# Kernel tuning notes

Hardware: AMD Instinct MI355X
Metric: run time of the kernel (lower is better)

Reference implementation:

```python
import jax, jax.numpy as jnp
import numpy as np

D = 64  # hidden_dim


def _bn(x, gamma, beta):
    # eval-mode BatchNorm1d with running_mean=0, running_var=1 (fresh model)
    return gamma * x + beta


def _edge_conv(h, W, b, gamma, beta):
    # h: [B,N,D]; W: [2D,D] split into Wi (acts on x_i) and Wj (acts on x_j)
    Wi, Wj = W[:D], W[D:]
    ti = jnp.einsum('bnd,de->bne', h, Wi)  # [B,N,D] (i term)
    tj = jnp.einsum('bmd,de->bme', h, Wj)  # [B,N,D] (j term)
    # e[b,i,j,:] = x_i@Wi + x_j@Wj + b  -> relu -> BN -> max over j
    e = ti[:, :, None, :] + tj[:, None, :, :] + b  # [B,N,N,D]
    e = _bn(jax.nn.relu(e), gamma, beta)
    return e.max(axis=2)  # [B,N,D]


def setup_inputs() -> dict:
    key = jax.random.key(0)
    ks = jax.random.split(key, 16)
    s = lambda k, shp, sc: (jax.random.normal(k, shp, dtype=jnp.float32) * sc)
    inp = {
        'x': s(ks[0], (32, 256, 4), 1.0),
        'W1': s(ks[1], (4, D), 0.5), 'b1': s(ks[2], (D,), 0.1),
        'g1': 1.0 + s(ks[3], (D,), 0.1), 'beta1': s(ks[4], (D,), 0.1),
        'We1': s(ks[5], (2 * D, D), 0.1), 'be1': s(ks[6], (D,), 0.1),
        'ge1': 1.0 + s(ks[7], (D,), 0.1), 'betae1': s(ks[8], (D,), 0.1),
        'We2': s(ks[9], (2 * D, D), 0.1), 'be2': s(ks[10], (D,), 0.1),
        'ge2': 1.0 + s(ks[11], (D,), 0.1), 'betae2': s(ks[12], (D,), 0.1),
        'Wg1': s(ks[13], (2 * D, D), 0.1), 'bg1': s(ks[14], (D,), 0.1),
        'Wg2': s(ks[15], (D, 2), 0.1), 'bg2': jnp.zeros((2,), jnp.float32),
    }
    return inp


def reference(x, W1, b1, g1, beta1, We1, be1, ge1, betae1, We2, be2, ge2, betae2, Wg1, bg1, Wg2, bg2):
    # input MLP: Linear -> ReLU -> BN (eval)
    h = _bn(jax.nn.relu(x @ W1 + b1), g1, beta1)  # [B,N,D]
    h = _edge_conv(h, We1, be1, ge1, betae1)
    h = _edge_conv(h, We2, be2, ge2, betae2)
    x_mean = h.mean(axis=1)  # [B,D]
    x_max = h.max(axis=1)    # [B,D]
    xg = jnp.concatenate([x_mean, x_max], axis=-1)  # [B,2D]
    # global MLP (dropout is identity in eval)
    out = jax.nn.relu(xg @ Wg1 + bg1) @ Wg2 + bg2  # [B,2]
    return out
```

## Files before the change

kernel.cpp:

```cpp
#include <hip/hip_runtime.h>

#define NB 32
#define NN 256
#define DD 64
#define GG 4
#define NPB 64
#define FMAXV 3.402823466e+38f


__global__ __launch_bounds__(512) void k_conv1(
    const float* __restrict__ x,
    const float* __restrict__ W1,  const float* __restrict__ b1,
    const float* __restrict__ g1,  const float* __restrict__ beta1,
    const float* __restrict__ We1,
    float* __restrict__ TI, float* __restrict__ PMAX, float* __restrict__ PMIN)
{
    __shared__ float Hs[NPB * 65];
    const int b  = blockIdx.x >> 2;
    const int g  = blockIdx.x & 3;
    const int l  = threadIdx.x & 63;
    const int w  = __builtin_amdgcn_readfirstlane(threadIdx.x >> 6);
    const int n  = g * NPB + l;
    const int d0 = w * 8;

    {
        float4 xv = *(const float4*)(x + ((size_t)b * NN + n) * 4);
        float a[8];
#pragma unroll
        for (int j = 0; j < 8; ++j) a[j] = b1[d0 + j];
#pragma unroll
        for (int j = 0; j < 8; ++j) a[j] = fmaf(xv.x, W1[0 * DD + d0 + j], a[j]);
#pragma unroll
        for (int j = 0; j < 8; ++j) a[j] = fmaf(xv.y, W1[1 * DD + d0 + j], a[j]);
#pragma unroll
        for (int j = 0; j < 8; ++j) a[j] = fmaf(xv.z, W1[2 * DD + d0 + j], a[j]);
#pragma unroll
        for (int j = 0; j < 8; ++j) a[j] = fmaf(xv.w, W1[3 * DD + d0 + j], a[j]);
#pragma unroll
        for (int j = 0; j < 8; ++j)
            Hs[l * 65 + d0 + j] = g1[d0 + j] * fmaxf(a[j], 0.f) + beta1[d0 + j];
    }
    __syncthreads();

    float ti[8], tj[8];
#pragma unroll
    for (int j = 0; j < 8; ++j) { ti[j] = 0.f; tj[j] = 0.f; }
#pragma unroll
    for (int k = 0; k < DD; ++k) {
        const float hk = Hs[l * 65 + k];
        const float* wi = We1 + k * DD + d0;
        const float* wj = We1 + (DD + k) * DD + d0;
#pragma unroll
        for (int j = 0; j < 8; ++j) {
            ti[j] = fmaf(hk, wi[j], ti[j]);
            tj[j] = fmaf(hk, wj[j], tj[j]);
        }
    }
    {
        float* o = TI + ((size_t)(b * NN + n)) * DD + d0;
        *(float4*)(o)     = make_float4(ti[0], ti[1], ti[2], ti[3]);
        *(float4*)(o + 4) = make_float4(ti[4], ti[5], ti[6], ti[7]);
    }
    float mx[8], mn[8];
#pragma unroll
    for (int j = 0; j < 8; ++j) { mx[j] = tj[j]; mn[j] = tj[j]; }
#pragma unroll
    for (int m = 1; m < 64; m <<= 1) {
#pragma unroll
        for (int j = 0; j < 8; ++j) {
            mx[j] = fmaxf(mx[j], __shfl_xor(mx[j], m, 64));
            mn[j] = fminf(mn[j], __shfl_xor(mn[j], m, 64));
        }
    }
    float smx = mx[0], smn = mn[0];
#pragma unroll
    for (int j = 1; j < 8; ++j) {
        smx = (l == j) ? mx[j] : smx;
        smn = (l == j) ? mn[j] : smn;
    }
    if (l < 8) {
        PMAX[(b * GG + g) * DD + d0 + l] = smx;
        PMIN[(b * GG + g) * DD + d0 + l] = smn;
    }
}

__global__ __launch_bounds__(512) void k_conv2(
    const float* __restrict__ PMAXin, const float* __restrict__ PMINin,
    const float* __restrict__ beP, const float* __restrict__ geP,
    const float* __restrict__ bteP,
    const float* __restrict__ We,
    float* __restrict__ TI, float* __restrict__ PMAX, float* __restrict__ PMIN)
{
    __shared__ float Hs[NPB * 65];
    const int b  = blockIdx.x >> 2;
    const int g  = blockIdx.x & 3;
    const int l  = threadIdx.x & 63;
    const int w  = __builtin_amdgcn_readfirstlane(threadIdx.x >> 6);
    const int n  = g * NPB + l;
    const int d0 = w * 8;

    float rmax[8], rmin[8];
#pragma unroll
    for (int j = 0; j < 8; ++j) {
        rmax[j] = fmaxf(fmaxf(PMAXin[(b * GG + 0) * DD + d0 + j],
                              PMAXin[(b * GG + 1) * DD + d0 + j]),
                        fmaxf(PMAXin[(b * GG + 2) * DD + d0 + j],
                              PMAXin[(b * GG + 3) * DD + d0 + j]));
        rmin[j] = fminf(fminf(PMINin[(b * GG + 0) * DD + d0 + j],
                              PMINin[(b * GG + 1) * DD + d0 + j]),
                        fminf(PMINin[(b * GG + 2) * DD + d0 + j],
                              PMINin[(b * GG + 3) * DD + d0 + j]));
    }
    {
        const float* tip = TI + ((size_t)(b * NN + n)) * DD + d0;
        float4 t0 = *(const float4*)tip;
        float4 t1 = *(const float4*)(tip + 4);
        float tiv[8] = {t0.x, t0.y, t0.z, t0.w, t1.x, t1.y, t1.z, t1.w};
#pragma unroll
        for (int j = 0; j < 8; ++j) {
            float gv = geP[d0 + j];
            float sv = tiv[j] + (gv >= 0.f ? rmax[j] : rmin[j]) + beP[d0 + j];
            Hs[l * 65 + d0 + j] = gv * fmaxf(sv, 0.f) + bteP[d0 + j];
        }
    }
    __syncthreads();

    float ti[8], tj[8];
#pragma unroll
    for (int j = 0; j < 8; ++j) { ti[j] = 0.f; tj[j] = 0.f; }
#pragma unroll
    for (int k = 0; k < DD; ++k) {
        const float hk = Hs[l * 65 + k];
        const float* wi = We + k * DD + d0;
        const float* wj = We + (DD + k) * DD + d0;
#pragma unroll
        for (int j = 0; j < 8; ++j) {
            ti[j] = fmaf(hk, wi[j], ti[j]);
            tj[j] = fmaf(hk, wj[j], tj[j]);
        }
    }
    {
        float* o = TI + ((size_t)(b * NN + n)) * DD + d0;
        *(float4*)(o)     = make_float4(ti[0], ti[1], ti[2], ti[3]);
        *(float4*)(o + 4) = make_float4(ti[4], ti[5], ti[6], ti[7]);
    }
    float mx[8], mn[8];
#pragma unroll
    for (int j = 0; j < 8; ++j) { mx[j] = tj[j]; mn[j] = tj[j]; }
#pragma unroll
    for (int m = 1; m < 64; m <<= 1) {
#pragma unroll
        for (int j = 0; j < 8; ++j) {
            mx[j] = fmaxf(mx[j], __shfl_xor(mx[j], m, 64));
            mn[j] = fminf(mn[j], __shfl_xor(mn[j], m, 64));
        }
    }
    float smx = mx[0], smn = mn[0];
#pragma unroll
    for (int j = 1; j < 8; ++j) {
        smx = (l == j) ? mx[j] : smx;
        smn = (l == j) ? mn[j] : smn;
    }
    if (l < 8) {
        PMAX[(b * GG + g) * DD + d0 + l] = smx;
        PMIN[(b * GG + g) * DD + d0 + l] = smn;
    }
}

__global__ __launch_bounds__(512) void k_pool(
    const float* __restrict__ PMAXin, const float* __restrict__ PMINin,
    const float* __restrict__ beP, const float* __restrict__ geP,
    const float* __restrict__ bteP,
    const float* __restrict__ TI,
    float* __restrict__ PSUM, float* __restrict__ PMXP)
{
    const int b  = blockIdx.x >> 2;
    const int g  = blockIdx.x & 3;
    const int l  = threadIdx.x & 63;
    const int w  = __builtin_amdgcn_readfirstlane(threadIdx.x >> 6);
    const int n  = g * NPB + l;
    const int d0 = w * 8;

    float rmax[8], rmin[8];
#pragma unroll
    for (int j = 0; j < 8; ++j) {
        rmax[j] = fmaxf(fmaxf(PMAXin[(b * GG + 0) * DD + d0 + j],
                              PMAXin[(b * GG + 1) * DD + d0 + j]),
                        fmaxf(PMAXin[(b * GG + 2) * DD + d0 + j],
                              PMAXin[(b * GG + 3) * DD + d0 + j]));
        rmin[j] = fminf(fminf(PMINin[(b * GG + 0) * DD + d0 + j],
                              PMINin[(b * GG + 1) * DD + d0 + j]),
                        fminf(PMINin[(b * GG + 2) * DD + d0 + j],
                              PMINin[(b * GG + 3) * DD + d0 + j]));
    }
    float hv[8];
    {
        const float* tip = TI + ((size_t)(b * NN + n)) * DD + d0;
        float4 t0 = *(const float4*)tip;
        float4 t1 = *(const float4*)(tip + 4);
        float tiv[8] = {t0.x, t0.y, t0.z, t0.w, t1.x, t1.y, t1.z, t1.w};
#pragma unroll
        for (int j = 0; j < 8; ++j) {
            float gv = geP[d0 + j];
            float sv = tiv[j] + (gv >= 0.f ? rmax[j] : rmin[j]) + beP[d0 + j];
            hv[j] = gv * fmaxf(sv, 0.f) + bteP[d0 + j];
        }
    }
    float sm[8], mx[8];
#pragma unroll
    for (int j = 0; j < 8; ++j) { sm[j] = hv[j]; mx[j] = hv[j]; }
#pragma unroll
    for (int m = 1; m < 64; m <<= 1) {
#pragma unroll
        for (int j = 0; j < 8; ++j) {
            sm[j] += __shfl_xor(sm[j], m, 64);
            mx[j] = fmaxf(mx[j], __shfl_xor(mx[j], m, 64));
        }
    }
    float ssm = sm[0], smx = mx[0];
#pragma unroll
    for (int j = 1; j < 8; ++j) {
        ssm = (l == j) ? sm[j] : ssm;
        smx = (l == j) ? mx[j] : smx;
    }
    if (l < 8) {
        PSUM[(b * GG + g) * DD + d0 + l] = ssm;
        PMXP[(b * GG + g) * DD + d0 + l] = smx;
    }
}

__global__ __launch_bounds__(128) void k_head(
    const float* __restrict__ PSUM, const float* __restrict__ PMXP,
    const float* __restrict__ Wg1, const float* __restrict__ bg1,
    const float* __restrict__ Wg2, const float* __restrict__ bg2,
    float* __restrict__ out)
{
    __shared__ float xg[2 * DD];
    __shared__ float hid[DD];
    const int b = blockIdx.x;
    const int t = threadIdx.x;
    if (t < 64) {
        float s = PSUM[(b * GG + 0) * DD + t] + PSUM[(b * GG + 1) * DD + t]
                + PSUM[(b * GG + 2) * DD + t] + PSUM[(b * GG + 3) * DD + t];
        xg[t] = s * (1.f / 256.f);
    } else {
        int d = t - 64;
        xg[64 + d] = fmaxf(fmaxf(PMXP[(b * GG + 0) * DD + d], PMXP[(b * GG + 1) * DD + d]),
                           fmaxf(PMXP[(b * GG + 2) * DD + d], PMXP[(b * GG + 3) * DD + d]));
    }
    __syncthreads();
    if (t < 64) {
        float a = bg1[t];
#pragma unroll
        for (int k = 0; k < 2 * DD; ++k) a = fmaf(xg[k], Wg1[k * DD + t], a);
        hid[t] = fmaxf(a, 0.f);
    }
    __syncthreads();
    if (t < 2) {
        float o = bg2[t];
#pragma unroll
        for (int j = 0; j < DD; ++j) o = fmaf(hid[j], Wg2[j * 2 + t], o);
        out[b * 2 + t] = o;
    }
}

extern "C" void kernel_launch(void* const* d_in, const int* in_sizes, int n_in,
                              void* d_out, int out_size, void* d_ws, size_t ws_size,
                              hipStream_t stream) {
    const float* x     = (const float*)d_in[0];
    const float* W1    = (const float*)d_in[1];
    const float* b1    = (const float*)d_in[2];
    const float* g1    = (const float*)d_in[3];
    const float* beta1 = (const float*)d_in[4];
    const float* We1   = (const float*)d_in[5];
    const float* be1   = (const float*)d_in[6];
    const float* ge1   = (const float*)d_in[7];
    const float* bte1  = (const float*)d_in[8];
    const float* We2   = (const float*)d_in[9];
    const float* be2   = (const float*)d_in[10];
    const float* ge2   = (const float*)d_in[11];
    const float* bte2  = (const float*)d_in[12];
    const float* Wg1   = (const float*)d_in[13];
    const float* bg1   = (const float*)d_in[14];
    const float* Wg2   = (const float*)d_in[15];
    const float* bg2   = (const float*)d_in[16];

    float* ws    = (float*)d_ws;
    float* TI    = ws;
    float* PMAX1 = ws + 524288;
    float* PMIN1 = ws + 532480;
    float* PMAX2 = ws + 540672;
    float* PMIN2 = ws + 548864;
    float* PSUM  = ws + 557056;
    float* PMXP  = ws + 565248;

    k_conv1<<<dim3(NB * GG), dim3(512), 0, stream>>>(
        x, W1, b1, g1, beta1, We1, TI, PMAX1, PMIN1);
    k_conv2<<<dim3(NB * GG), dim3(512), 0, stream>>>(
        PMAX1, PMIN1, be1, ge1, bte1, We2, TI, PMAX2, PMIN2);
    k_pool<<<dim3(NB * GG), dim3(512), 0, stream>>>(
        PMAX2, PMIN2, be2, ge2, bte2, TI, PSUM, PMXP);
    k_head<<<dim3(NB), dim3(128), 0, stream>>>(
        PSUM, PMXP, Wg1, bg1, Wg2, bg2, (float*)d_out);
}
```

Baseline: 121.4 us.

## Fuse all stages into one cooperative kernel with grid syncs

Replaces four separate kernel launches with a single cooperative kernel that uses grid-wide synchronization between stages. The per-node ti term stays in registers across stages instead of round-tripping through the TI workspace buffer. This removes launch gaps and global traffic, but adds grid.sync costs and requires all 128 blocks to be co-resident.

```diff
diff --git a/kernel.cpp b/kernel.cpp
--- a/kernel.cpp
+++ b/kernel.cpp
@@ -1,27 +1,48 @@
 #include <hip/hip_runtime.h>
+#include <hip/hip_cooperative_groups.h>
+
+namespace cg = cooperative_groups;
 
 #define NB 32
 #define NN 256
 #define DD 64
 #define GG 4
 #define NPB 64
-#define FMAXV 3.402823466e+38f
-
-
-__global__ __launch_bounds__(512) void k_conv1(
+#define NBLK (NB * GG)
+
+
+__global__ __launch_bounds__(512, 1) void pnet_coop(
     const float* __restrict__ x,
     const float* __restrict__ W1,  const float* __restrict__ b1,
     const float* __restrict__ g1,  const float* __restrict__ beta1,
-    const float* __restrict__ We1,
-    float* __restrict__ TI, float* __restrict__ PMAX, float* __restrict__ PMIN)
+    const float* __restrict__ We1, const float* __restrict__ be1,
+    const float* __restrict__ ge1, const float* __restrict__ bte1,
+    const float* __restrict__ We2, const float* __restrict__ be2,
+    const float* __restrict__ ge2, const float* __restrict__ bte2,
+    const float* __restrict__ Wg1, const float* __restrict__ bg1,
+    const float* __restrict__ Wg2, const float* __restrict__ bg2,
+    float* __restrict__ PM, float* __restrict__ out)
 {
+    cg::grid_group grid = cg::this_grid();
+
     __shared__ float Hs[NPB * 65];
-    const int b  = blockIdx.x >> 2;
-    const int g  = blockIdx.x & 3;
-    const int l  = threadIdx.x & 63;
-    const int w  = __builtin_amdgcn_readfirstlane(threadIdx.x >> 6);
-    const int n  = g * NPB + l;
-    const int d0 = w * 8;
+    __shared__ float XG[2 * DD];
+    __shared__ float HID[DD];
+
+    float* PMAX1 = PM;
+    float* PMIN1 = PM + 8192;
+    float* PMAX2 = PM + 16384;
+    float* PMIN2 = PM + 24576;
+    float* PSUM  = PM + 32768;
+    float* PMXP  = PM + 40960;
+
+    const int bid = blockIdx.x;
+    const int b   = bid >> 2;
+    const int g   = bid & 3;
+    const int l   = threadIdx.x & 63;
+    const int w   = __builtin_amdgcn_readfirstlane(threadIdx.x >> 6);
+    const int n   = g * NPB + l;
+    const int d0  = w * 8;
 
     {
         float4 xv = *(const float4*)(x + ((size_t)b * NN + n) * 4);
@@ -42,225 +63,176 @@
     }
     __syncthreads();
 
-    float ti[8], tj[8];
-#pragma unroll
-    for (int j = 0; j < 8; ++j) { ti[j] = 0.f; tj[j] = 0.f; }
-#pragma unroll
-    for (int k = 0; k < DD; ++k) {
-        const float hk = Hs[l * 65 + k];
-        const float* wi = We1 + k * DD + d0;
-        const float* wj = We1 + (DD + k) * DD + d0;
-#pragma unroll
-        for (int j = 0; j < 8; ++j) {
-            ti[j] = fmaf(hk, wi[j], ti[j]);
-            tj[j] = fmaf(hk, wj[j], tj[j]);
-        }
-    }
-    {
-        float* o = TI + ((size_t)(b * NN + n)) * DD + d0;
-        *(float4*)(o)     = make_float4(ti[0], ti[1], ti[2], ti[3]);
-        *(float4*)(o + 4) = make_float4(ti[4], ti[5], ti[6], ti[7]);
-    }
-    float mx[8], mn[8];
-#pragma unroll
-    for (int j = 0; j < 8; ++j) { mx[j] = tj[j]; mn[j] = tj[j]; }
-#pragma unroll
-    for (int m = 1; m < 64; m <<= 1) {
-#pragma unroll
-        for (int j = 0; j < 8; ++j) {
-            mx[j] = fmaxf(mx[j], __shfl_xor(mx[j], m, 64));
-            mn[j] = fminf(mn[j], __shfl_xor(mn[j], m, 64));
-        }
-    }
-    float smx = mx[0], smn = mn[0];
-#pragma unroll
-    for (int j = 1; j < 8; ++j) {
-        smx = (l == j) ? mx[j] : smx;
-        smn = (l == j) ? mn[j] : smn;
-    }
-    if (l < 8) {
-        PMAX[(b * GG + g) * DD + d0 + l] = smx;
-        PMIN[(b * GG + g) * DD + d0 + l] = smn;
-    }
-}
-
-__global__ __launch_bounds__(512) void k_conv2(
-    const float* __restrict__ PMAXin, const float* __restrict__ PMINin,
-    const float* __restrict__ beP, const float* __restrict__ geP,
-    const float* __restrict__ bteP,
-    const float* __restrict__ We,
-    float* __restrict__ TI, float* __restrict__ PMAX, float* __restrict__ PMIN)
-{
-    __shared__ float Hs[NPB * 65];
-    const int b  = blockIdx.x >> 2;
-    const int g  = blockIdx.x & 3;
-    const int l  = threadIdx.x & 63;
-    const int w  = __builtin_amdgcn_readfirstlane(threadIdx.x >> 6);
-    const int n  = g * NPB + l;
-    const int d0 = w * 8;
-
-    float rmax[8], rmin[8];
-#pragma unroll
-    for (int j = 0; j < 8; ++j) {
-        rmax[j] = fmaxf(fmaxf(PMAXin[(b * GG + 0) * DD + d0 + j],
-                              PMAXin[(b * GG + 1) * DD + d0 + j]),
-                        fmaxf(PMAXin[(b * GG + 2) * DD + d0 + j],
-                              PMAXin[(b * GG + 3) * DD + d0 + j]));
-        rmin[j] = fminf(fminf(PMINin[(b * GG + 0) * DD + d0 + j],
-                              PMINin[(b * GG + 1) * DD + d0 + j]),
-                        fminf(PMINin[(b * GG + 2) * DD + d0 + j],
-                              PMINin[(b * GG + 3) * DD + d0 + j]));
-    }
-    {
-        const float* tip = TI + ((size_t)(b * NN + n)) * DD + d0;
-        float4 t0 = *(const float4*)tip;
-        float4 t1 = *(const float4*)(tip + 4);
-        float tiv[8] = {t0.x, t0.y, t0.z, t0.w, t1.x, t1.y, t1.z, t1.w};
-#pragma unroll
-        for (int j = 0; j < 8; ++j) {
-            float gv = geP[d0 + j];
-            float sv = tiv[j] + (gv >= 0.f ? rmax[j] : rmin[j]) + beP[d0 + j];
-            Hs[l * 65 + d0 + j] = gv * fmaxf(sv, 0.f) + bteP[d0 + j];
-        }
-    }
-    __syncthreads();
-
-    float ti[8], tj[8];
-#pragma unroll
-    for (int j = 0; j < 8; ++j) { ti[j] = 0.f; tj[j] = 0.f; }
-#pragma unroll
-    for (int k = 0; k < DD; ++k) {
-        const float hk = Hs[l * 65 + k];
-        const float* wi = We + k * DD + d0;
-        const float* wj = We + (DD + k) * DD + d0;
-#pragma unroll
-        for (int j = 0; j < 8; ++j) {
-            ti[j] = fmaf(hk, wi[j], ti[j]);
-            tj[j] = fmaf(hk, wj[j], tj[j]);
-        }
-    }
-    {
-        float* o = TI + ((size_t)(b * NN + n)) * DD + d0;
-        *(float4*)(o)     = make_float4(ti[0], ti[1], ti[2], ti[3]);
-        *(float4*)(o + 4) = make_float4(ti[4], ti[5], ti[6], ti[7]);
-    }
-    float mx[8], mn[8];
-#pragma unroll
-    for (int j = 0; j < 8; ++j) { mx[j] = tj[j]; mn[j] = tj[j]; }
-#pragma unroll
-    for (int m = 1; m < 64; m <<= 1) {
-#pragma unroll
-        for (int j = 0; j < 8; ++j) {
-            mx[j] = fmaxf(mx[j], __shfl_xor(mx[j], m, 64));
-            mn[j] = fminf(mn[j], __shfl_xor(mn[j], m, 64));
-        }
-    }
-    float smx = mx[0], smn = mn[0];
-#pragma unroll
-    for (int j = 1; j < 8; ++j) {
-        smx = (l == j) ? mx[j] : smx;
-        smn = (l == j) ? mn[j] : smn;
-    }
-    if (l < 8) {
-        PMAX[(b * GG + g) * DD + d0 + l] = smx;
-        PMIN[(b * GG + g) * DD + d0 + l] = smn;
-    }
-}
-
-__global__ __launch_bounds__(512) void k_pool(
-    const float* __restrict__ PMAXin, const float* __restrict__ PMINin,
-    const float* __restrict__ beP, const float* __restrict__ geP,
-    const float* __restrict__ bteP,
-    const float* __restrict__ TI,
-    float* __restrict__ PSUM, float* __restrict__ PMXP)
-{
-    const int b  = blockIdx.x >> 2;
-    const int g  = blockIdx.x & 3;
-    const int l  = threadIdx.x & 63;
-    const int w  = __builtin_amdgcn_readfirstlane(threadIdx.x >> 6);
-    const int n  = g * NPB + l;
-    const int d0 = w * 8;
-
-    float rmax[8], rmin[8];
-#pragma unroll
-    for (int j = 0; j < 8; ++j) {
-        rmax[j] = fmaxf(fmaxf(PMAXin[(b * GG + 0) * DD + d0 + j],
-                              PMAXin[(b * GG + 1) * DD + d0 + j]),
-                        fmaxf(PMAXin[(b * GG + 2) * DD + d0 + j],
-                              PMAXin[(b * GG + 3) * DD + d0 + j]));
-        rmin[j] = fminf(fminf(PMINin[(b * GG + 0) * DD + d0 + j],
-                              PMINin[(b * GG + 1) * DD + d0 + j]),
-                        fminf(PMINin[(b * GG + 2) * DD + d0 + j],
-                              PMINin[(b * GG + 3) * DD + d0 + j]));
-    }
-    float hv[8];
-    {
-        const float* tip = TI + ((size_t)(b * NN + n)) * DD + d0;
-        float4 t0 = *(const float4*)tip;
-        float4 t1 = *(const float4*)(tip + 4);
-        float tiv[8] = {t0.x, t0.y, t0.z, t0.w, t1.x, t1.y, t1.z, t1.w};
-#pragma unroll
-        for (int j = 0; j < 8; ++j) {
-            float gv = geP[d0 + j];
-            float sv = tiv[j] + (gv >= 0.f ? rmax[j] : rmin[j]) + beP[d0 + j];
-            hv[j] = gv * fmaxf(sv, 0.f) + bteP[d0 + j];
-        }
-    }
-    float sm[8], mx[8];
-#pragma unroll
-    for (int j = 0; j < 8; ++j) { sm[j] = hv[j]; mx[j] = hv[j]; }
-#pragma unroll
-    for (int m = 1; m < 64; m <<= 1) {
-#pragma unroll
-        for (int j = 0; j < 8; ++j) {
-            sm[j] += __shfl_xor(sm[j], m, 64);
-            mx[j] = fmaxf(mx[j], __shfl_xor(mx[j], m, 64));
-        }
-    }
-    float ssm = sm[0], smx = mx[0];
-#pragma unroll
-    for (int j = 1; j < 8; ++j) {
-        ssm = (l == j) ? sm[j] : ssm;
-        smx = (l == j) ? mx[j] : smx;
-    }
-    if (l < 8) {
-        PSUM[(b * GG + g) * DD + d0 + l] = ssm;
-        PMXP[(b * GG + g) * DD + d0 + l] = smx;
-    }
-}
-
-__global__ __launch_bounds__(128) void k_head(
-    const float* __restrict__ PSUM, const float* __restrict__ PMXP,
-    const float* __restrict__ Wg1, const float* __restrict__ bg1,
-    const float* __restrict__ Wg2, const float* __restrict__ bg2,
-    float* __restrict__ out)
-{
-    __shared__ float xg[2 * DD];
-    __shared__ float hid[DD];
-    const int b = blockIdx.x;
-    const int t = threadIdx.x;
-    if (t < 64) {
-        float s = PSUM[(b * GG + 0) * DD + t] + PSUM[(b * GG + 1) * DD + t]
-                + PSUM[(b * GG + 2) * DD + t] + PSUM[(b * GG + 3) * DD + t];
-        xg[t] = s * (1.f / 256.f);
-    } else {
-        int d = t - 64;
-        xg[64 + d] = fmaxf(fmaxf(PMXP[(b * GG + 0) * DD + d], PMXP[(b * GG + 1) * DD + d]),
-                           fmaxf(PMXP[(b * GG + 2) * DD + d], PMXP[(b * GG + 3) * DD + d]));
-    }
-    __syncthreads();
-    if (t < 64) {
-        float a = bg1[t];
-#pragma unroll
-        for (int k = 0; k < 2 * DD; ++k) a = fmaf(xg[k], Wg1[k * DD + t], a);
-        hid[t] = fmaxf(a, 0.f);
-    }
-    __syncthreads();
-    if (t < 2) {
-        float o = bg2[t];
-#pragma unroll
-        for (int j = 0; j < DD; ++j) o = fmaf(hid[j], Wg2[j * 2 + t], o);
-        out[b * 2 + t] = o;
+    float ti1[8];
+    {
+        float tj[8];
+#pragma unroll
+        for (int j = 0; j < 8; ++j) { ti1[j] = 0.f; tj[j] = 0.f; }
+#pragma unroll
+        for (int k = 0; k < DD; ++k) {
+            const float hk = Hs[l * 65 + k];
+            const float* wi = We1 + k * DD + d0;
+            const float* wj = We1 + (DD + k) * DD + d0;
+#pragma unroll
+            for (int j = 0; j < 8; ++j) {
+                ti1[j] = fmaf(hk, wi[j], ti1[j]);
+                tj[j]  = fmaf(hk, wj[j], tj[j]);
+            }
+        }
+        float mx[8], mn[8];
+#pragma unroll
+        for (int j = 0; j < 8; ++j) { mx[j] = tj[j]; mn[j] = tj[j]; }
+#pragma unroll
+        for (int m = 1; m < 64; m <<= 1) {
+#pragma unroll
+            for (int j = 0; j < 8; ++j) {
+                mx[j] = fmaxf(mx[j], __shfl_xor(mx[j], m, 64));
+                mn[j] = fminf(mn[j], __shfl_xor(mn[j], m, 64));
+            }
+        }
+        float smx = mx[0], smn = mn[0];
+#pragma unroll
+        for (int j = 1; j < 8; ++j) {
+            smx = (l == j) ? mx[j] : smx;
+            smn = (l == j) ? mn[j] : smn;
+        }
+        if (l < 8) {
+            PMAX1[(b * GG + g) * DD + d0 + l] = smx;
+            PMIN1[(b * GG + g) * DD + d0 + l] = smn;
+        }
+    }
+    grid.sync();
+
+    float ti2[8];
+    {
+        float rmax[8], rmin[8];
+#pragma unroll
+        for (int j = 0; j < 8; ++j) {
+            rmax[j] = fmaxf(fmaxf(PMAX1[(b * GG + 0) * DD + d0 + j],
+                                  PMAX1[(b * GG + 1) * DD + d0 + j]),
+                            fmaxf(PMAX1[(b * GG + 2) * DD + d0 + j],
+                                  PMAX1[(b * GG + 3) * DD + d0 + j]));
+            rmin[j] = fminf(fminf(PMIN1[(b * GG + 0) * DD + d0 + j],
+                                  PMIN1[(b * GG + 1) * DD + d0 + j]),
+                            fminf(PMIN1[(b * GG + 2) * DD + d0 + j],
+                                  PMIN1[(b * GG + 3) * DD + d0 + j]));
+        }
+        __syncthreads();
+#pragma unroll
+        for (int j = 0; j < 8; ++j) {
+            float gv = ge1[d0 + j];
+            float sv = ti1[j] + (gv >= 0.f ? rmax[j] : rmin[j]) + be1[d0 + j];
+            Hs[l * 65 + d0 + j] = gv * fmaxf(sv, 0.f) + bte1[d0 + j];
+        }
+        __syncthreads();
+
+        float tj[8];
+#pragma unroll
+        for (int j = 0; j < 8; ++j) { ti2[j] = 0.f; tj[j] = 0.f; }
+#pragma unroll
+        for (int k = 0; k < DD; ++k) {
+            const float hk = Hs[l * 65 + k];
+            const float* wi = We2 + k * DD + d0;
+            const float* wj = We2 + (DD + k) * DD + d0;
+#pragma unroll
+            for (int j = 0; j < 8; ++j) {
+                ti2[j] = fmaf(hk, wi[j], ti2[j]);
+                tj[j]  = fmaf(hk, wj[j], tj[j]);
+            }
+        }
+        float mx[8], mn[8];
+#pragma unroll
+        for (int j = 0; j < 8; ++j) { mx[j] = tj[j]; mn[j] = tj[j]; }
+#pragma unroll
+        for (int m = 1; m < 64; m <<= 1) {
+#pragma unroll
+            for (int j = 0; j < 8; ++j) {
+                mx[j] = fmaxf(mx[j], __shfl_xor(mx[j], m, 64));
+                mn[j] = fminf(mn[j], __shfl_xor(mn[j], m, 64));
+            }
+        }
+        float smx = mx[0], smn = mn[0];
+#pragma unroll
+        for (int j = 1; j < 8; ++j) {
+            smx = (l == j) ? mx[j] : smx;
+            smn = (l == j) ? mn[j] : smn;
+        }
+        if (l < 8) {
+            PMAX2[(b * GG + g) * DD + d0 + l] = smx;
+            PMIN2[(b * GG + g) * DD + d0 + l] = smn;
+        }
+    }
+    grid.sync();
+
+    {
+        float rmax[8], rmin[8];
+#pragma unroll
+        for (int j = 0; j < 8; ++j) {
+            rmax[j] = fmaxf(fmaxf(PMAX2[(b * GG + 0) * DD + d0 + j],
+                                  PMAX2[(b * GG + 1) * DD + d0 + j]),
+                            fmaxf(PMAX2[(b * GG + 2) * DD + d0 + j],
+                                  PMAX2[(b * GG + 3) * DD + d0 + j]));
+            rmin[j] = fminf(fminf(PMIN2[(b * GG + 0) * DD + d0 + j],
+                                  PMIN2[(b * GG + 1) * DD + d0 + j]),
+                            fminf(PMIN2[(b * GG + 2) * DD + d0 + j],
+                                  PMIN2[(b * GG + 3) * DD + d0 + j]));
+        }
+        float hv[8];
+#pragma unroll
+        for (int j = 0; j < 8; ++j) {
+            float gv = ge2[d0 + j];
+            float sv = ti2[j] + (gv >= 0.f ? rmax[j] : rmin[j]) + be2[d0 + j];
+            hv[j] = gv * fmaxf(sv, 0.f) + bte2[d0 + j];
+        }
+        float sm[8], mx[8];
+#pragma unroll
+        for (int j = 0; j < 8; ++j) { sm[j] = hv[j]; mx[j] = hv[j]; }
+#pragma unroll
+        for (int m = 1; m < 64; m <<= 1) {
+#pragma unroll
+            for (int j = 0; j < 8; ++j) {
+                sm[j] += __shfl_xor(sm[j], m, 64);
+                mx[j] = fmaxf(mx[j], __shfl_xor(mx[j], m, 64));
+            }
+        }
+        float ssm = sm[0], smx = mx[0];
+#pragma unroll
+        for (int j = 1; j < 8; ++j) {
+            ssm = (l == j) ? sm[j] : ssm;
+            smx = (l == j) ? mx[j] : smx;
+        }
+        if (l < 8) {
+            PSUM[(b * GG + g) * DD + d0 + l] = ssm;
+            PMXP[(b * GG + g) * DD + d0 + l] = smx;
+        }
+    }
+    grid.sync();
+
+    if (g == 0) {
+        const int t = threadIdx.x;
+        if (t < 64) {
+            float s = PSUM[(b * GG + 0) * DD + t] + PSUM[(b * GG + 1) * DD + t]
+                    + PSUM[(b * GG + 2) * DD + t] + PSUM[(b * GG + 3) * DD + t];
+            XG[t] = s * (1.f / 256.f);
+        } else if (t < 128) {
+            int d = t - 64;
+            XG[64 + d] = fmaxf(fmaxf(PMXP[(b * GG + 0) * DD + d], PMXP[(b * GG + 1) * DD + d]),
+                               fmaxf(PMXP[(b * GG + 2) * DD + d], PMXP[(b * GG + 3) * DD + d]));
+        }
+        __syncthreads();
+        if (t < 64) {
+            float a = bg1[t];
+#pragma unroll
+            for (int k = 0; k < 2 * DD; ++k) a = fmaf(XG[k], Wg1[k * DD + t], a);
+            HID[t] = fmaxf(a, 0.f);
+        }
+        __syncthreads();
+        if (t < 2) {
+            float o = bg2[t];
+#pragma unroll
+            for (int j = 0; j < DD; ++j) o = fmaf(HID[j], Wg2[j * 2 + t], o);
+            out[b * 2 + t] = o;
+        }
     }
 }
 
@@ -284,22 +256,16 @@
     const float* bg1   = (const float*)d_in[14];
     const float* Wg2   = (const float*)d_in[15];
     const float* bg2   = (const float*)d_in[16];
-
-    float* ws    = (float*)d_ws;
-    float* TI    = ws;
-    float* PMAX1 = ws + 524288;
-    float* PMIN1 = ws + 532480;
-    float* PMAX2 = ws + 540672;
-    float* PMIN2 = ws + 548864;
-    float* PSUM  = ws + 557056;
-    float* PMXP  = ws + 565248;
-
-    k_conv1<<<dim3(NB * GG), dim3(512), 0, stream>>>(
-        x, W1, b1, g1, beta1, We1, TI, PMAX1, PMIN1);
-    k_conv2<<<dim3(NB * GG), dim3(512), 0, stream>>>(
-        PMAX1, PMIN1, be1, ge1, bte1, We2, TI, PMAX2, PMIN2);
-    k_pool<<<dim3(NB * GG), dim3(512), 0, stream>>>(
-        PMAX2, PMIN2, be2, ge2, bte2, TI, PSUM, PMXP);
-    k_head<<<dim3(NB), dim3(128), 0, stream>>>(
-        PSUM, PMXP, Wg1, bg1, Wg2, bg2, (float*)d_out);
+    float* PM  = (float*)d_ws;
+    float* out = (float*)d_out;
+
+    void* args[] = {
+        (void*)&x, (void*)&W1, (void*)&b1, (void*)&g1, (void*)&beta1,
+        (void*)&We1, (void*)&be1, (void*)&ge1, (void*)&bte1,
+        (void*)&We2, (void*)&be2, (void*)&ge2, (void*)&bte2,
+        (void*)&Wg1, (void*)&bg1, (void*)&Wg2, (void*)&bg2,
+        (void*)&PM, (void*)&out
+    };
+    hipLaunchCooperativeKernel((void*)pnet_coop, dim3(NBLK), dim3(512),
+                               args, 0, stream);
 }
```

Measured after the change: 204.0 us. +68.1%, slower.

## Fuse pooling and head MLP into one per-batch kernel with LDS reduction

Applied to the files above, without the earlier changes.

Merges the pooling kernel and the global MLP head into a single kernel launched with one block per batch instead of four. Each thread now computes 32 channels for one point and writes them to a padded shared-memory tile, which is then reduced by columns for sum and max before the head MLP runs in the same block. This removes one kernel launch and the global round trip for the partial sums. In exchange it runs only 32 blocks with large shared memory and more registers per thread, so much less of the GPU is occupied.

```diff
diff --git a/kernel.cpp b/kernel.cpp
--- a/kernel.cpp
+++ b/kernel.cpp
@@ -5,7 +5,6 @@
 #define DD 64
 #define GG 4
 #define NPB 64
-#define FMAXV 3.402823466e+38f
 
 
 __global__ __launch_bounds__(512) void k_conv1(
@@ -167,23 +166,32 @@
     }
 }
 
-__global__ __launch_bounds__(512) void k_pool(
+__global__ __launch_bounds__(512, 1) void k_poolhead(
     const float* __restrict__ PMAXin, const float* __restrict__ PMINin,
     const float* __restrict__ beP, const float* __restrict__ geP,
     const float* __restrict__ bteP,
     const float* __restrict__ TI,
-    float* __restrict__ PSUM, float* __restrict__ PMXP)
+    const float* __restrict__ Wg1, const float* __restrict__ bg1,
+    const float* __restrict__ Wg2, const float* __restrict__ bg2,
+    float* __restrict__ out)
 {
-    const int b  = blockIdx.x >> 2;
-    const int g  = blockIdx.x & 3;
-    const int l  = threadIdx.x & 63;
-    const int w  = __builtin_amdgcn_readfirstlane(threadIdx.x >> 6);
-    const int n  = g * NPB + l;
-    const int d0 = w * 8;
-
-    float rmax[8], rmin[8];
-#pragma unroll
-    for (int j = 0; j < 8; ++j) {
+    __shared__ float TT[2 * NN * 33];
+    __shared__ float PA[8 * 64];
+    __shared__ float PB[8 * 64];
+    __shared__ float XG[2 * DD];
+    __shared__ float HID[DD];
+
+    const int b  = blockIdx.x;
+    const int t  = threadIdx.x;
+    const int l  = t & 63;
+    const int w  = __builtin_amdgcn_readfirstlane(t >> 6);
+    const int s2 = w >> 2;
+    const int n  = (w & 3) * 64 + l;
+    const int d0 = s2 * 32;
+
+    float rmax[32], rmin[32];
+#pragma unroll
+    for (int j = 0; j < 32; ++j) {
         rmax[j] = fmaxf(fmaxf(PMAXin[(b * GG + 0) * DD + d0 + j],
                               PMAXin[(b * GG + 1) * DD + d0 + j]),
                         fmaxf(PMAXin[(b * GG + 2) * DD + d0 + j],
@@ -193,73 +201,64 @@
                         fminf(PMINin[(b * GG + 2) * DD + d0 + j],
                               PMINin[(b * GG + 3) * DD + d0 + j]));
     }
-    float hv[8];
+
     {
         const float* tip = TI + ((size_t)(b * NN + n)) * DD + d0;
-        float4 t0 = *(const float4*)tip;
-        float4 t1 = *(const float4*)(tip + 4);
-        float tiv[8] = {t0.x, t0.y, t0.z, t0.w, t1.x, t1.y, t1.z, t1.w};
-#pragma unroll
-        for (int j = 0; j < 8; ++j) {
-            float gv = geP[d0 + j];
-            float sv = tiv[j] + (gv >= 0.f ? rmax[j] : rmin[j]) + beP[d0 + j];
-            hv[j] = gv * fmaxf(sv, 0.f) + bteP[d0 + j];
-        }
-    }
-    float sm[8], mx[8];
-#pragma unroll
-    for (int j = 0; j < 8; ++j) { sm[j] = hv[j]; mx[j] = hv[j]; }
-#pragma unroll
-    for (int m = 1; m < 64; m <<= 1) {
-#pragma unroll
-        for (int j = 0; j < 8; ++j) {
-            sm[j] += __shfl_xor(sm[j], m, 64);
-            mx[j] = fmaxf(mx[j], __shfl_xor(mx[j], m, 64));
-        }
-    }
-    float ssm = sm[0], smx = mx[0];
-#pragma unroll
-    for (int j = 1; j < 8; ++j) {
-        ssm = (l == j) ? sm[j] : ssm;
-        smx = (l == j) ? mx[j] : smx;
-    }
-    if (l < 8) {
-        PSUM[(b * GG + g) * DD + d0 + l] = ssm;
-        PMXP[(b * GG + g) * DD + d0 + l] = smx;
-    }
-}
-
-__global__ __launch_bounds__(128) void k_head(
-    const float* __restrict__ PSUM, const float* __restrict__ PMXP,
-    const float* __restrict__ Wg1, const float* __restrict__ bg1,
-    const float* __restrict__ Wg2, const float* __restrict__ bg2,
-    float* __restrict__ out)
-{
-    __shared__ float xg[2 * DD];
-    __shared__ float hid[DD];
-    const int b = blockIdx.x;
-    const int t = threadIdx.x;
+        float* Tw = TT + (s2 * NN + n) * 33;
+#pragma unroll
+        for (int j4 = 0; j4 < 8; ++j4) {
+            float4 tv = ((const float4*)tip)[j4];
+            float tvv[4] = {tv.x, tv.y, tv.z, tv.w};
+#pragma unroll
+            for (int q = 0; q < 4; ++q) {
+                int j = 4 * j4 + q;
+                float gv = geP[d0 + j];
+                float sv = tvv[q] + (gv >= 0.f ? rmax[j] : rmin[j]) + beP[d0 + j];
+                Tw[j] = gv * fmaxf(sv, 0.f) + bteP[d0 + j];
+            }
+        }
+    }
+    __syncthreads();
+
+    {
+        const int d   = t & 63;
+        const int grp = t >> 6;
+        const int ss  = d >> 5;
+        const int jj  = d & 31;
+        float sm = 0.f, mx = -3.402823466e+38f;
+#pragma unroll
+        for (int m = 0; m < 32; ++m) {
+            float v = TT[(ss * NN + grp * 32 + m) * 33 + jj];
+            sm += v;
+            mx = fmaxf(mx, v);
+        }
+        PA[grp * 64 + d] = sm;
+        PB[grp * 64 + d] = mx;
+    }
+    __syncthreads();
     if (t < 64) {
-        float s = PSUM[(b * GG + 0) * DD + t] + PSUM[(b * GG + 1) * DD + t]
-                + PSUM[(b * GG + 2) * DD + t] + PSUM[(b * GG + 3) * DD + t];
-        xg[t] = s * (1.f / 256.f);
-    } else {
-        int d = t - 64;
-        xg[64 + d] = fmaxf(fmaxf(PMXP[(b * GG + 0) * DD + d], PMXP[(b * GG + 1) * DD + d]),
-                           fmaxf(PMXP[(b * GG + 2) * DD + d], PMXP[(b * GG + 3) * DD + d]));
-    }
-    __syncthreads();
+        float asum = PA[t], amax = PB[t];
+#pragma unroll
+        for (int q = 1; q < 8; ++q) {
+            asum += PA[q * 64 + t];
+            amax = fmaxf(amax, PB[q * 64 + t]);
+        }
+        XG[t]      = asum * (1.f / 256.f);
+        XG[64 + t] = amax;
+    }
+    __syncthreads();
+
     if (t < 64) {
         float a = bg1[t];
 #pragma unroll
-        for (int k = 0; k < 2 * DD; ++k) a = fmaf(xg[k], Wg1[k * DD + t], a);
-        hid[t] = fmaxf(a, 0.f);
+        for (int k = 0; k < 2 * DD; ++k) a = fmaf(XG[k], Wg1[k * DD + t], a);
+        HID[t] = fmaxf(a, 0.f);
     }
     __syncthreads();
     if (t < 2) {
         float o = bg2[t];
 #pragma unroll
-        for (int j = 0; j < DD; ++j) o = fmaf(hid[j], Wg2[j * 2 + t], o);
+        for (int j = 0; j < DD; ++j) o = fmaf(HID[j], Wg2[j * 2 + t], o);
         out[b * 2 + t] = o;
     }
 }
@@ -291,15 +290,11 @@
     float* PMIN1 = ws + 532480;
     float* PMAX2 = ws + 540672;
     float* PMIN2 = ws + 548864;
-    float* PSUM  = ws + 557056;
-    float* PMXP  = ws + 565248;
 
     k_conv1<<<dim3(NB * GG), dim3(512), 0, stream>>>(
         x, W1, b1, g1, beta1, We1, TI, PMAX1, PMIN1);
     k_conv2<<<dim3(NB * GG), dim3(512), 0, stream>>>(
         PMAX1, PMIN1, be1, ge1, bte1, We2, TI, PMAX2, PMIN2);
-    k_pool<<<dim3(NB * GG), dim3(512), 0, stream>>>(
-        PMAX2, PMIN2, be2, ge2, bte2, TI, PSUM, PMXP);
-    k_head<<<dim3(NB), dim3(128), 0, stream>>>(
-        PSUM, PMXP, Wg1, bg1, Wg2, bg2, (float*)d_out);
+    k_poolhead<<<dim3(NB), dim3(512), 0, stream>>>(
+        PMAX2, PMIN2, be2, ge2, bte2, TI, Wg1, bg1, Wg2, bg2, (float*)d_out);
 }
```

New measurement: 123.2 us. Within noise of the previous version (+1.5%).
